# Performance work log

Hardware: AMD Instinct MI355X
Metric: run time of the kernel (lower is better)

## Reference

```python
import jax, jax.numpy as jnp
import numpy as np
from jax import lax

# pywt db5 analysis filter bank (frozen buffers in the torch module)
DEC_LO = np.array([0.003335725285001549, -0.012580751999015526, -0.006241490213011705,
                   0.07757149384006515, -0.03224486958502952, -0.24229488706619015,
                   0.13842814590110342, 0.7243085284385744, 0.6038292697974729,
                   0.160102397974125], dtype=np.float32)
DEC_HI = np.array([-0.160102397974125, 0.6038292697974729, -0.7243085284385744,
                   0.13842814590110342, 0.24229488706619015, -0.03224486958502952,
                   -0.07757149384006515, -0.006241490213011705, 0.012580751999015526,
                   0.003335725285001549], dtype=np.float32)
NUM_LEVELS = 8  # min(round(log2(131072)), max_level=8)


def _conv1d(x, w, padding, lhs_dilation=(1,), groups=1):
    # x: [N, C, L], w: [O, I, K]; cross-correlation, matching torch F.conv1d
    return lax.conv_general_dilated(
        x, w, window_strides=(1,), padding=[padding], lhs_dilation=lhs_dilation,
        dimension_numbers=("NCH", "OIH", "NCH"), feature_group_count=groups)


def setup_inputs() -> dict:
    key = jax.random.key(0)
    k1, k2 = jax.random.split(key)
    x = jax.random.normal(k1, (128, 131072), dtype=jnp.float32)
    # small scale keeps the 8-level synthesis cascade numerically tame
    idwt_filters = jax.random.normal(k2, (128, 8, 2, 32), dtype=jnp.float32) * 0.05
    return {"x": x, "idwt_filters": idwt_filters}


def reference(x, idwt_filters):
    # x: [B, T]; idwt_filters: [B, levels, 2, kw] with kw even
    B, T = x.shape
    w_lo = jnp.asarray(DEC_LO).reshape(1, 1, -1)
    w_hi = jnp.asarray(DEC_HI).reshape(1, 1, -1)
    pad = DEC_LO.shape[0] // 2  # 5 -> conv output length L+1 for kernel 10

    # --- analysis DWT (frozen db5 filters), lengths: T/2^l + 1 per band ---
    lo = x[:, None, :]                       # [B,1,T]
    his = []
    for _ in range(NUM_LEVELS):
        y_lo = _conv1d(lo, w_lo, (pad, pad))
        y_hi = _conv1d(lo, w_hi, (pad, pad))
        lo = y_lo[:, :, ::2]
        his.append(y_hi[:, :, ::2])          # [B,1,T/2^l+1]

    # --- synthesis IDWT with predicted per-example filters (groups=B) ---
    kw = idwt_filters.shape[-1]
    p = kw // 2 - 1
    prev = jnp.transpose(lo, (1, 0, 2))      # [1,B,n]: batch as channels
    for i in range(NUM_LEVELS - 1, -1, -1):
        rec_lo = idwt_filters[:, i, 0, :][:, None, :]   # [B,1,kw]
        rec_hi = idwt_filters[:, i, 1, :][:, None, :]
        hi = jnp.transpose(his[i], (1, 0, 2))           # [1,B,n]
        # lhs_dilation=2 == zero-stuffing even indices; asym pad (p, p+1)
        # reproduces torch's trailing zero at index 2n-1; out length = 2n-1
        y_lo = _conv1d(prev, rec_lo, (p, p + 1), lhs_dilation=(2,), groups=B)
        y_hi = _conv1d(hi, rec_hi, (p, p + 1), lhs_dilation=(2,), groups=B)
        prev = y_lo + y_hi
    return prev[0, :, :-1]                   # [B, T]
```

## Files before the change

### kernel.cpp

```cpp
#include <hip/hip_runtime.h>


static __constant__ float c_dec_lo[10] = {
    0.003335725285001549f, -0.012580751999015526f, -0.006241490213011705f,
    0.07757149384006515f, -0.03224486958502952f, -0.24229488706619015f,
    0.13842814590110342f, 0.7243085284385744f, 0.6038292697974729f,
    0.160102397974125f};
static __constant__ float c_dec_hi[10] = {
    -0.160102397974125f, 0.6038292697974729f, -0.7243085284385744f,
    0.13842814590110342f, 0.24229488706619015f, -0.03224486958502952f,
    -0.07757149384006515f, -0.006241490213011705f, 0.012580751999015526f,
    0.003335725285001549f};

__device__ inline float4 ldz4(const float* __restrict__ row, int j, int L) {
  if (j >= 0 && j + 3 < L) return *reinterpret_cast<const float4*>(row + j);
  float4 r;
  r.x = (j + 0 >= 0 && j + 0 < L) ? row[j + 0] : 0.f;
  r.y = (j + 1 >= 0 && j + 1 < L) ? row[j + 1] : 0.f;
  r.z = (j + 2 >= 0 && j + 2 < L) ? row[j + 2] : 0.f;
  r.w = (j + 3 >= 0 && j + 3 < L) ? row[j + 3] : 0.f;
  return r;
}

__device__ inline void load20(const float* src, int base, float* v) {
#pragma unroll
  for (int q = 0; q < 5; ++q) {
    const float4 t = *reinterpret_cast<const float4*>(src + base + 4 * q);
    v[4 * q + 0] = t.x; v[4 * q + 1] = t.y;
    v[4 * q + 2] = t.z; v[4 * q + 3] = t.w;
  }
}

__device__ inline void load20z(const float* __restrict__ src, int base, int L,
                               float* v) {
#pragma unroll
  for (int q = 0; q < 5; ++q) {
    const float4 t = ldz4(src, base + 4 * q, L);
    v[4 * q + 0] = t.x; v[4 * q + 1] = t.y;
    v[4 * q + 2] = t.z; v[4 * q + 3] = t.w;
  }
}

__device__ inline void load12(const float* src, float* v) {
#pragma unroll
  for (int q = 0; q < 3; ++q) {
    const float4 t = *reinterpret_cast<const float4*>(src + 4 * q);
    v[4 * q + 0] = t.x; v[4 * q + 1] = t.y;
    v[4 * q + 2] = t.z; v[4 * q + 3] = t.w;
  }
}

__device__ inline void fir10x2(const float* v, float* lo, float* hv) {
#pragma unroll
  for (int i = 0; i < 4; ++i) {
    float a = 0.f, h = 0.f;
#pragma unroll
    for (int k = 0; k < 10; ++k) {
      const float xx = v[2 * i + 3 + k];
      a += xx * c_dec_lo[k];
      h += xx * c_dec_hi[k];
    }
    lo[i] = a; hv[i] = h;
  }
}

__device__ inline void fir10x2_split(const float* e, const float* o,
                                     float* lo, float* hv) {
#pragma unroll
  for (int i = 0; i < 4; ++i) {
    float a = 0.f, h = 0.f;
#pragma unroll
    for (int m = 0; m < 5; ++m) {
      const float ov = o[i + 1 + m], ev = e[i + 2 + m];
      a += ov * c_dec_lo[2 * m] + ev * c_dec_lo[2 * m + 1];
      h += ov * c_dec_hi[2 * m] + ev * c_dec_hi[2 * m + 1];
    }
    lo[i] = a; hv[i] = h;
  }
}

__device__ inline void store_hi(float* hg, int A, int idx, const float* hv,
                                int es, int ee) {
  if (idx >= es && idx + 3 < ee) {
    *reinterpret_cast<float4*>(hg + A + idx) =
        make_float4(hv[0], hv[1], hv[2], hv[3]);
  } else {
#pragma unroll
    for (int i = 0; i < 4; ++i)
      if (idx + i >= es && idx + i < ee) hg[A + idx + i] = hv[i];
  }
}

__device__ inline void st4(float* dst, const float* a) {
  *reinterpret_cast<float4*>(dst) = make_float4(a[0], a[1], a[2], a[3]);
}

__device__ inline void store_pad_split(float* E, float* O, int idx,
                                       const float* lo, int vlo, int vhi) {
#pragma unroll
  for (int i = 0; i < 4; ++i) {
    const int s = idx + i;
    const float val = (s >= vlo && s < vhi) ? lo[i] : 0.f;
    if (s & 1) O[s >> 1] = val;
    else E[s >> 1] = val;
  }
}

template <bool FAST>
__device__ inline void fwd_level0(const float* __restrict__ xr, float* E0,
                                  float* O0, float* __restrict__ h0, int A0,
                                  int xoff, int vlo, int vhi, int tid) {
  const int ee = FAST ? 4152 : min(4152, vhi);
  for (int idx = 4 * tid; idx < 4180; idx += 1024) {
    float v[20];
    if (FAST) load20(xr, 2 * idx + xoff, v);
    else load20z(xr, 2 * idx + xoff, 131072, v);
    float lo[4], hv[4];
    fir10x2(v, lo, hv);
    if (FAST) {
      const int j = idx >> 1;
      *reinterpret_cast<float2*>(E0 + j) = make_float2(lo[0], lo[2]);
      *reinterpret_cast<float2*>(O0 + j) = make_float2(lo[1], lo[3]);
      if (idx >= 56 && idx < 4152) st4(h0 + A0 + idx, hv);
    } else {
      store_pad_split(E0, O0, idx, lo, vlo, vhi);
      store_hi(h0, A0, idx, hv, 56, ee);
    }
  }
}

template <bool FAST>
__device__ inline void fwd_levelN(const float* Ein, const float* Oin,
                                  float* Eout, float* Oout,
                                  float* __restrict__ hg, int A, int NOUT,
                                  int esHi, int eeFast, int vlo, int vhi,
                                  int tid) {
  const int ee = FAST ? eeFast : min(eeFast, vhi);
  for (int idx = 4 * tid; idx < NOUT; idx += 1024) {
    float e[12], o[12];
    load12(Ein + idx, e);
    load12(Oin + idx, o);
    float lo[4], hv[4];
    fir10x2_split(e, o, lo, hv);
    if (FAST) {
      const int j = idx >> 1;
      *reinterpret_cast<float2*>(Eout + j) = make_float2(lo[0], lo[2]);
      *reinterpret_cast<float2*>(Oout + j) = make_float2(lo[1], lo[3]);
      if (idx >= esHi && idx < ee) st4(hg + A + idx, hv);
    } else {
      store_pad_split(Eout, Oout, idx, lo, vlo, vhi);
      store_hi(hg, A, idx, hv, esHi, ee);
    }
  }
}

template <bool FAST>
__device__ inline void fwd_level3(const float* Ein, const float* Oin,
                                  float* __restrict__ l3,
                                  float* __restrict__ h3, int b3, int ne3,
                                  int tid) {
  for (int idx = 4 * tid; idx < 512; idx += 1024) {
    float e[12], o[12];
    load12(Ein + idx, e);
    load12(Oin + idx, o);
    float lo[4], hv[4];
    fir10x2_split(e, o, lo, hv);
    if (FAST) {
      st4(l3 + b3 + idx, lo);
      st4(h3 + b3 + idx, hv);
    } else {
      store_hi(l3, b3, idx, lo, 0, ne3);
      store_hi(h3, b3, idx, hv, 0, ne3);
    }
  }
}

__global__ __launch_bounds__(256) void fwd03(
    const float* __restrict__ x, float* __restrict__ hi0,
    float* __restrict__ hi1, float* __restrict__ hi2,
    float* __restrict__ hi3, float* __restrict__ lo3) {
  const int b = blockIdx.y;
  const int bx = blockIdx.x;
  const int b3 = bx * 512;
  __shared__ float E0[2092], O0[2092];
  __shared__ float E1[1044], O1[1044];
  __shared__ float E2[520], O2[520];
  const int tid = threadIdx.x;
  const bool fast = (bx >= 1) && (bx <= 14);
  const float* xr = x + (size_t)b * 131072;
  float* h0 = hi0 + (size_t)b * 65540;
  float* h1 = hi1 + (size_t)b * 32772;
  float* h2 = hi2 + (size_t)b * 16388;
  float* h3 = hi3 + (size_t)b * 8196;
  float* l3 = lo3 + (size_t)b * 8196;
  const int A0 = 8 * b3 - 56, A1 = 4 * b3 - 24, A2 = 2 * b3 - 8;
  const int xoff = 2 * A0 - 8;

  if (fast) {
    fwd_level0<true>(xr, E0, O0, h0, A0, xoff, 0, 0, tid);
    __syncthreads();
    fwd_levelN<true>(E0, O0, E1, O1, h1, A1, 2084, 24, 2072, 0, 0, tid);
    __syncthreads();
    fwd_levelN<true>(E1, O1, E2, O2, h2, A2, 1036, 8, 1032, 0, 0, tid);
    __syncthreads();
    fwd_level3<true>(E2, O2, l3, h3, b3, 512, tid);
  } else {
    fwd_level0<false>(xr, E0, O0, h0, A0, xoff, -A0, 65537 - A0, tid);
    __syncthreads();
    fwd_levelN<false>(E0, O0, E1, O1, h1, A1, 2084, 24, 2072, -A1,
                      32769 - A1, tid);
    __syncthreads();
    fwd_levelN<false>(E1, O1, E2, O2, h2, A2, 1036, 8, 1032, -A2, 16385 - A2,
                      tid);
    __syncthreads();
    fwd_level3<false>(E2, O2, l3, h3, b3, min(512, 8193 - b3), tid);
  }
}

__device__ inline void inv_accum(const float* p, const float* h,
                                 const float4* wpk, float* acc) {
#pragma unroll
  for (int i = 0; i < 8; ++i) acc[i] = 0.f;
#pragma unroll
  for (int m = 0; m < 16; ++m) {
    const float4 w = wpk[m];
#pragma unroll
    for (int e = 0; e < 4; ++e) {
      const float pe = p[e + 1 + m], he = h[e + 1 + m];
      acc[2 * e + 0] += pe * w.y + he * w.w;
      acc[2 * e + 1] += pe * w.x + he * w.z;
    }
  }
}

__global__ __launch_bounds__(256) void inv_big(
    const float* __restrict__ prev, const float* __restrict__ hicoef,
    const float* __restrict__ filt, int level, int L, int sIn, int Tout,
    int sOut, float* __restrict__ out) {
  const int c = blockIdx.y;
  __shared__ float4 wpack[16];
  const int tid = threadIdx.x;
  if (tid < 16) {
    const float* f = filt + ((size_t)c * 8 + level) * 64;
    wpack[tid] = make_float4(f[2 * tid], f[2 * tid + 1],
                             f[32 + 2 * tid], f[32 + 2 * tid + 1]);
  }
  __syncthreads();
  const int g = blockIdx.x * 256 + tid;
  const int t0 = 16 * g;
  if (t0 >= Tout) return;
  const int U = 8 * g - 8;
  const float* prow = prev + (size_t)c * sIn;
  const float* hrow = hicoef + (size_t)c * sIn;
  float p[24], h[24];
  const bool interior = (U >= 0) && (U + 23 < L) && (t0 + 15 < Tout);
  if (interior) {
#pragma unroll
    for (int q = 0; q < 6; ++q) {
      float4 a = *reinterpret_cast<const float4*>(prow + U + 4 * q);
      p[4 * q + 0] = a.x; p[4 * q + 1] = a.y; p[4 * q + 2] = a.z; p[4 * q + 3] = a.w;
      float4 bb = *reinterpret_cast<const float4*>(hrow + U + 4 * q);
      h[4 * q + 0] = bb.x; h[4 * q + 1] = bb.y; h[4 * q + 2] = bb.z; h[4 * q + 3] = bb.w;
    }
  } else {
#pragma unroll
    for (int q = 0; q < 24; ++q) {
      const int j = U + q;
      p[q] = (j >= 0 && j < L) ? prow[j] : 0.f;
      h[q] = (j >= 0 && j < L) ? hrow[j] : 0.f;
    }
  }
  float acc[16];
#pragma unroll
  for (int i = 0; i < 16; ++i) acc[i] = 0.f;
#pragma unroll
  for (int m = 0; m < 16; ++m) {
    const float4 w = wpack[m];
#pragma unroll
    for (int e = 0; e < 8; ++e) {
      const float pv = p[e + 1 + m], hv = h[e + 1 + m];
      acc[2 * e + 0] += pv * w.y + hv * w.w;
      acc[2 * e + 1] += pv * w.x + hv * w.z;
    }
  }
  float* orow = out + (size_t)c * sOut;
  if (interior) {
#pragma unroll
    for (int q = 0; q < 4; ++q)
      *reinterpret_cast<float4*>(orow + t0 + 4 * q) =
          make_float4(acc[4 * q], acc[4 * q + 1], acc[4 * q + 2], acc[4 * q + 3]);
  } else {
#pragma unroll
    for (int i = 0; i < 16; ++i)
      if (t0 + i < Tout) orow[t0 + i] = acc[i];
  }
}

__device__ inline void fwd_tail_level(const float* __restrict__ in,
                                      float* __restrict__ outp, int L, int D,
                                      float* __restrict__ hirow, int tid) {
  for (int d0 = 4 * tid; d0 < D; d0 += 2048) {
    const int jb = 2 * d0 - 8;
    float v[20];
    const bool interior = (jb >= 0) && (jb + 19 < L) && (d0 + 3 < D);
    if (interior) {
      load20(in, jb, v);
    } else {
#pragma unroll
      for (int q = 0; q < 20; ++q) {
        const int j = jb + q;
        v[q] = (j >= 0 && j < L) ? in[j] : 0.f;
      }
    }
    float lo[4], hv[4];
    fir10x2(v, lo, hv);
    if (interior) {
      st4(outp + d0, lo);
      st4(hirow + d0, hv);
    } else {
#pragma unroll
      for (int i = 0; i < 4; ++i)
        if (d0 + i < D) { outp[d0 + i] = lo[i]; hirow[d0 + i] = hv[i]; }
    }
  }
}

__device__ inline void inv_tail_level(const float* __restrict__ pin,
                                      float* __restrict__ pout, int L,
                                      const float* __restrict__ hirow,
                                      const float* __restrict__ filt, int c,
                                      int level, int tid, float4* wpack) {
  __syncthreads();
  if (tid < 16) {
    const float* f = filt + ((size_t)c * 8 + level) * 64;
    wpack[tid] = make_float4(f[2 * tid], f[2 * tid + 1], f[32 + 2 * tid],
                             f[32 + 2 * tid + 1]);
  }
  __syncthreads();
  const int Tout = 2 * L - 1;
  for (int t0 = 8 * tid; t0 < Tout; t0 += 4096) {
    const int U = t0 / 2 - 8;
    float p[20], h[20];
    if (U >= 0 && U + 19 < L) {
      load20(pin, U, p);
      load20(hirow, U, h);
    } else {
#pragma unroll
      for (int q = 0; q < 20; ++q) {
        const int j = U + q;
        p[q] = (j >= 0 && j < L) ? pin[j] : 0.f;
        h[q] = (j >= 0 && j < L) ? hirow[j] : 0.f;
      }
    }
    float acc[8];
    inv_accum(p, h, wpack, acc);
    if (t0 + 7 < Tout) {
      st4(pout + t0, acc);
      st4(pout + t0 + 4, acc + 4);
    } else {
#pragma unroll
      for (int i = 0; i < 8; ++i)
        if (t0 + i < Tout) pout[t0 + i] = acc[i];
    }
  }
}

__global__ __launch_bounds__(512) void mid_fused(
    const float* __restrict__ lo3, const float* __restrict__ filt,
    float* __restrict__ prev3out) {
  const int b = blockIdx.x;
  __shared__ float A[8200];
  __shared__ float Bb[4104];
  __shared__ float H4[4100];
  __shared__ float H5[2052];
  __shared__ float H6[1028];
  __shared__ float H7[516];
  __shared__ float4 wpack[16];
  const int tid = threadIdx.x;
  const float* row = lo3 + (size_t)b * 8196;
  for (int j4 = tid; j4 < 2048; j4 += 512)
    *reinterpret_cast<float4*>(A + 4 * j4) =
        *reinterpret_cast<const float4*>(row + 4 * j4);
  if (tid == 0) A[8192] = row[8192];
  __syncthreads();
  fwd_tail_level(A, Bb, 8193, 4097, H4, tid);
  __syncthreads();
  fwd_tail_level(Bb, A, 4097, 2049, H5, tid);
  __syncthreads();
  fwd_tail_level(A, Bb, 2049, 1025, H6, tid);
  __syncthreads();
  fwd_tail_level(Bb, A, 1025, 513, H7, tid);
  inv_tail_level(A, Bb, 513, H7, filt, b, 7, tid, wpack);
  inv_tail_level(Bb, A, 1025, H6, filt, b, 6, tid, wpack);
  inv_tail_level(A, Bb, 2049, H5, filt, b, 5, tid, wpack);
  inv_tail_level(Bb, prev3out + (size_t)b * 8196, 4097, H4, filt, b, 4, tid,
                 wpack);
}

extern "C" void kernel_launch(void* const* d_in, const int* in_sizes, int n_in,
                              void* d_out, int out_size, void* d_ws,
                              size_t ws_size, hipStream_t stream) {
  const float* x = (const float*)d_in[0];
  const float* filt = (const float*)d_in[1];
  float* out = (float*)d_out;
  float* ws = (float*)d_ws;

  const int B = 128;
  float* lo3buf = ws;
  float* prev3buf = lo3buf + (size_t)B * 8196;
  float* hi0 = prev3buf + (size_t)B * 8196;
  float* hi1 = hi0 + (size_t)B * 65540;
  float* hi2 = hi1 + (size_t)B * 32772;
  float* hi3 = hi2 + (size_t)B * 16388;
  float* prev2buf = hi3 + (size_t)B * 8196;
  float* prev1buf = prev2buf + (size_t)B * 16388;
  float* prev0buf = prev1buf + (size_t)B * 32772;

  hipLaunchKernelGGL(fwd03, dim3(17, B), dim3(256), 0, stream, x, hi0, hi1,
                     hi2, hi3, lo3buf);
  hipLaunchKernelGGL(mid_fused, dim3(B), dim3(512), 0, stream, lo3buf, filt,
                     prev3buf);

  auto launch_inv = [&](const float* prev, const float* hv, int level, int L,
                        int sIn, int Tout, int sOut, float* dst) {
    const int tpr = (Tout + 15) / 16;
    dim3 grid((tpr + 255) / 256, B);
    hipLaunchKernelGGL(inv_big, grid, dim3(256), 0, stream, prev, hv, filt,
                       level, L, sIn, Tout, sOut, dst);
  };
  launch_inv(prev3buf, hi3, 3, 8193, 8196, 16385, 16388, prev2buf);
  launch_inv(prev2buf, hi2, 2, 16385, 16388, 32769, 32772, prev1buf);
  launch_inv(prev1buf, hi1, 1, 32769, 32772, 65537, 65540, prev0buf);
  launch_inv(prev0buf, hi0, 0, 65537, 65540, 131072, 131072, out);
}
```

Measured before the change: 133.4 us.

## Stage input into shared memory and halve forward tile per block

```diff
diff --git a/kernel.cpp b/kernel.cpp
--- a/kernel.cpp
+++ b/kernel.cpp
@@ -31,16 +31,6 @@
   }
 }
 
-__device__ inline void load20z(const float* __restrict__ src, int base, int L,
-                               float* v) {
-#pragma unroll
-  for (int q = 0; q < 5; ++q) {
-    const float4 t = ldz4(src, base + 4 * q, L);
-    v[4 * q + 0] = t.x; v[4 * q + 1] = t.y;
-    v[4 * q + 2] = t.z; v[4 * q + 3] = t.w;
-  }
-}
-
 __device__ inline void load12(const float* src, float* v) {
 #pragma unroll
   for (int q = 0; q < 3; ++q) {
@@ -107,25 +97,14 @@
 }
 
 template <bool FAST>
-__device__ inline void fwd_level0(const float* __restrict__ xr, float* E0,
-                                  float* O0, float* __restrict__ h0, int A0,
-                                  int xoff, int vlo, int vhi, int tid) {
-  const int ee = FAST ? 4152 : min(4152, vhi);
-  for (int idx = 4 * tid; idx < 4180; idx += 1024) {
-    float v[20];
-    if (FAST) load20(xr, 2 * idx + xoff, v);
-    else load20z(xr, 2 * idx + xoff, 131072, v);
-    float lo[4], hv[4];
-    fir10x2(v, lo, hv);
-    if (FAST) {
-      const int j = idx >> 1;
-      *reinterpret_cast<float2*>(E0 + j) = make_float2(lo[0], lo[2]);
-      *reinterpret_cast<float2*>(O0 + j) = make_float2(lo[1], lo[3]);
-      if (idx >= 56 && idx < 4152) st4(h0 + A0 + idx, hv);
-    } else {
-      store_pad_split(E0, O0, idx, lo, vlo, vhi);
-      store_hi(h0, A0, idx, hv, 56, ee);
-    }
+__device__ inline void stage_x(const float* __restrict__ xr, float* Ex,
+                               float* Ox, int xlo, int tid) {
+  for (int u = tid; u < 1069; u += 256) {
+    const float4 v = FAST
+        ? *reinterpret_cast<const float4*>(xr + xlo + 4 * u)
+        : ldz4(xr, xlo + 4 * u, 131072);
+    *reinterpret_cast<float2*>(Ex + 2 * u) = make_float2(v.x, v.z);
+    *reinterpret_cast<float2*>(Ox + 2 * u) = make_float2(v.y, v.w);
   }
 }
 
@@ -159,7 +138,7 @@
                                   float* __restrict__ l3,
                                   float* __restrict__ h3, int b3, int ne3,
                                   int tid) {
-  for (int idx = 4 * tid; idx < 512; idx += 1024) {
+  for (int idx = 4 * tid; idx < 256; idx += 1024) {
     float e[12], o[12];
     load12(Ein + idx, e);
     load12(Oin + idx, o);
@@ -181,12 +160,18 @@
     float* __restrict__ hi3, float* __restrict__ lo3) {
   const int b = blockIdx.y;
   const int bx = blockIdx.x;
-  const int b3 = bx * 512;
-  __shared__ float E0[2092], O0[2092];
-  __shared__ float E1[1044], O1[1044];
-  __shared__ float E2[520], O2[520];
+  const int b3 = bx * 256;
+  __shared__ float W[6416];
+  float* Ex = W;
+  float* Ox = W + 2140;
+  float* E0 = W + 4280;
+  float* O0 = W + 5348;
+  float* E1 = W;
+  float* O1 = W + 532;
+  float* E2 = W + 1064;
+  float* O2 = W + 1328;
   const int tid = threadIdx.x;
-  const bool fast = (bx >= 1) && (bx <= 14);
+  const bool fast = (bx >= 1) && (bx <= 30);
   const float* xr = x + (size_t)b * 131072;
   float* h0 = hi0 + (size_t)b * 65540;
   float* h1 = hi1 + (size_t)b * 32772;
@@ -194,26 +179,31 @@
   float* h3 = hi3 + (size_t)b * 8196;
   float* l3 = lo3 + (size_t)b * 8196;
   const int A0 = 8 * b3 - 56, A1 = 4 * b3 - 24, A2 = 2 * b3 - 8;
-  const int xoff = 2 * A0 - 8;
+  const int xlo = 2 * A0 - 8;
 
   if (fast) {
-    fwd_level0<true>(xr, E0, O0, h0, A0, xoff, 0, 0, tid);
-    __syncthreads();
-    fwd_levelN<true>(E0, O0, E1, O1, h1, A1, 2084, 24, 2072, 0, 0, tid);
-    __syncthreads();
-    fwd_levelN<true>(E1, O1, E2, O2, h2, A2, 1036, 8, 1032, 0, 0, tid);
-    __syncthreads();
-    fwd_level3<true>(E2, O2, l3, h3, b3, 512, tid);
+    stage_x<true>(xr, Ex, Ox, xlo, tid);
+    __syncthreads();
+    fwd_levelN<true>(Ex, Ox, E0, O0, h0, A0, 2132, 56, 2104, 0, 0, tid);
+    __syncthreads();
+    fwd_levelN<true>(E0, O0, E1, O1, h1, A1, 1060, 24, 1048, 0, 0, tid);
+    __syncthreads();
+    fwd_levelN<true>(E1, O1, E2, O2, h2, A2, 524, 8, 520, 0, 0, tid);
+    __syncthreads();
+    fwd_level3<true>(E2, O2, l3, h3, b3, 256, tid);
   } else {
-    fwd_level0<false>(xr, E0, O0, h0, A0, xoff, -A0, 65537 - A0, tid);
-    __syncthreads();
-    fwd_levelN<false>(E0, O0, E1, O1, h1, A1, 2084, 24, 2072, -A1,
+    stage_x<false>(xr, Ex, Ox, xlo, tid);
+    __syncthreads();
+    fwd_levelN<false>(Ex, Ox, E0, O0, h0, A0, 2132, 56, 2104, -A0,
+                      65537 - A0, tid);
+    __syncthreads();
+    fwd_levelN<false>(E0, O0, E1, O1, h1, A1, 1060, 24, 1048, -A1,
                       32769 - A1, tid);
     __syncthreads();
-    fwd_levelN<false>(E1, O1, E2, O2, h2, A2, 1036, 8, 1032, -A2, 16385 - A2,
+    fwd_levelN<false>(E1, O1, E2, O2, h2, A2, 524, 8, 520, -A2, 16385 - A2,
                       tid);
     __syncthreads();
-    fwd_level3<false>(E2, O2, l3, h3, b3, min(512, 8193 - b3), tid);
+    fwd_level3<false>(E2, O2, l3, h3, b3, min(256, 8193 - b3), tid);
   }
 }
 
@@ -416,7 +406,7 @@
   float* prev1buf = prev2buf + (size_t)B * 16388;
   float* prev0buf = prev1buf + (size_t)B * 32772;
 
-  hipLaunchKernelGGL(fwd03, dim3(17, B), dim3(256), 0, stream, x, hi0, hi1,
+  hipLaunchKernelGGL(fwd03, dim3(33, B), dim3(256), 0, stream, x, hi0, hi1,
                      hi2, hi3, lo3buf);
   hipLaunchKernelGGL(mid_fused, dim3(B), dim3(512), 0, stream, lo3buf, filt,
                      prev3buf);
```

New measurement: 134.6 us. About the same (+0.9%).

## Split forward DWT levels 0-3 into independent per-wave tiles with wave-level sync

Applied to the files above, without the earlier changes.

```diff
diff --git a/kernel.cpp b/kernel.cpp
--- a/kernel.cpp
+++ b/kernel.cpp
@@ -106,72 +106,84 @@
   }
 }
 
+__device__ inline void wave_sync() {
+  __builtin_amdgcn_wave_barrier();
+  asm volatile("s_waitcnt lgkmcnt(0)" ::: "memory");
+  __builtin_amdgcn_wave_barrier();
+}
+
 template <bool FAST>
-__device__ inline void fwd_level0(const float* __restrict__ xr, float* E0,
-                                  float* O0, float* __restrict__ h0, int A0,
-                                  int xoff, int vlo, int vhi, int tid) {
-  const int ee = FAST ? 4152 : min(4152, vhi);
-  for (int idx = 4 * tid; idx < 4180; idx += 1024) {
-    float v[20];
-    if (FAST) load20(xr, 2 * idx + xoff, v);
-    else load20z(xr, 2 * idx + xoff, 131072, v);
-    float lo[4], hv[4];
-    fir10x2(v, lo, hv);
-    if (FAST) {
-      const int j = idx >> 1;
-      *reinterpret_cast<float2*>(E0 + j) = make_float2(lo[0], lo[2]);
-      *reinterpret_cast<float2*>(O0 + j) = make_float2(lo[1], lo[3]);
-      if (idx >= 56 && idx < 4152) st4(h0 + A0 + idx, hv);
-    } else {
-      store_pad_split(E0, O0, idx, lo, vlo, vhi);
-      store_hi(h0, A0, idx, hv, 56, ee);
+__device__ inline void wl_level0(const float* __restrict__ xr, float* E0,
+                                 float* O0, float* __restrict__ h0, int A0,
+                                 int xoff, int vlo, int vhi, int eeh,
+                                 int lane) {
+#pragma unroll
+  for (int i = 0; i < 5; ++i) {
+    const int idx = 4 * lane + 256 * i;
+    if (idx < 1108) {
+      float v[20];
+      if (FAST) load20(xr, 2 * idx + xoff, v);
+      else load20z(xr, 2 * idx + xoff, 131072, v);
+      float lo[4], hv[4];
+      fir10x2(v, lo, hv);
+      if (FAST) {
+        const int j = idx >> 1;
+        *reinterpret_cast<float2*>(E0 + j) = make_float2(lo[0], lo[2]);
+        *reinterpret_cast<float2*>(O0 + j) = make_float2(lo[1], lo[3]);
+        if (idx >= 56 && idx < 1080) st4(h0 + A0 + idx, hv);
+      } else {
+        store_pad_split(E0, O0, idx, lo, vlo, vhi);
+        store_hi(h0, A0, idx, hv, 56, eeh);
+      }
     }
   }
 }
 
 template <bool FAST>
-__device__ inline void fwd_levelN(const float* Ein, const float* Oin,
-                                  float* Eout, float* Oout,
-                                  float* __restrict__ hg, int A, int NOUT,
-                                  int esHi, int eeFast, int vlo, int vhi,
-                                  int tid) {
-  const int ee = FAST ? eeFast : min(eeFast, vhi);
-  for (int idx = 4 * tid; idx < NOUT; idx += 1024) {
-    float e[12], o[12];
-    load12(Ein + idx, e);
-    load12(Oin + idx, o);
-    float lo[4], hv[4];
-    fir10x2_split(e, o, lo, hv);
-    if (FAST) {
-      const int j = idx >> 1;
-      *reinterpret_cast<float2*>(Eout + j) = make_float2(lo[0], lo[2]);
-      *reinterpret_cast<float2*>(Oout + j) = make_float2(lo[1], lo[3]);
-      if (idx >= esHi && idx < ee) st4(hg + A + idx, hv);
-    } else {
-      store_pad_split(Eout, Oout, idx, lo, vlo, vhi);
-      store_hi(hg, A, idx, hv, esHi, ee);
+__device__ inline void wl_levelN(const float* Ein, const float* Oin,
+                                 float* Eout, float* Oout,
+                                 float* __restrict__ hg, int A, int NOUT,
+                                 int iters, int esHi, int eeHiF, int vlo,
+                                 int vhi, int lane) {
+  for (int i = 0; i < iters; ++i) {
+    const int idx = 4 * lane + 256 * i;
+    if (idx < NOUT) {
+      float e[12], o[12];
+      load12(Ein + idx, e);
+      load12(Oin + idx, o);
+      float lo[4], hv[4];
+      fir10x2_split(e, o, lo, hv);
+      if (FAST) {
+        const int j = idx >> 1;
+        *reinterpret_cast<float2*>(Eout + j) = make_float2(lo[0], lo[2]);
+        *reinterpret_cast<float2*>(Oout + j) = make_float2(lo[1], lo[3]);
+        if (idx >= esHi && idx < eeHiF) st4(hg + A + idx, hv);
+      } else {
+        store_pad_split(Eout, Oout, idx, lo, vlo, vhi);
+        store_hi(hg, A, idx, hv, esHi, min(eeHiF, vhi));
+      }
     }
   }
 }
 
 template <bool FAST>
-__device__ inline void fwd_level3(const float* Ein, const float* Oin,
-                                  float* __restrict__ l3,
-                                  float* __restrict__ h3, int b3, int ne3,
-                                  int tid) {
-  for (int idx = 4 * tid; idx < 512; idx += 1024) {
-    float e[12], o[12];
-    load12(Ein + idx, e);
-    load12(Oin + idx, o);
-    float lo[4], hv[4];
-    fir10x2_split(e, o, lo, hv);
-    if (FAST) {
-      st4(l3 + b3 + idx, lo);
-      st4(h3 + b3 + idx, hv);
-    } else {
-      store_hi(l3, b3, idx, lo, 0, ne3);
-      store_hi(h3, b3, idx, hv, 0, ne3);
-    }
+__device__ inline void wl_level3(const float* Ein, const float* Oin,
+                                 float* __restrict__ l3,
+                                 float* __restrict__ h3, int T, int ne3,
+                                 int lane) {
+  const int idx = 4 * lane;
+  if (idx >= 128) return;
+  float e[12], o[12];
+  load12(Ein + idx, e);
+  load12(Oin + idx, o);
+  float lo[4], hv[4];
+  fir10x2_split(e, o, lo, hv);
+  if (FAST) {
+    st4(l3 + T + idx, lo);
+    st4(h3 + T + idx, hv);
+  } else {
+    store_hi(l3, T, idx, lo, 0, ne3);
+    store_hi(h3, T, idx, hv, 0, ne3);
   }
 }
 
@@ -180,40 +192,46 @@
     float* __restrict__ hi1, float* __restrict__ hi2,
     float* __restrict__ hi3, float* __restrict__ lo3) {
   const int b = blockIdx.y;
-  const int bx = blockIdx.x;
-  const int b3 = bx * 512;
-  __shared__ float E0[2092], O0[2092];
-  __shared__ float E1[1044], O1[1044];
-  __shared__ float E2[520], O2[520];
-  const int tid = threadIdx.x;
-  const bool fast = (bx >= 1) && (bx <= 14);
+  const int widx = threadIdx.x >> 6;
+  const int lane = threadIdx.x & 63;
+  const int gw = blockIdx.x * 4 + widx;
+  __shared__ float W[7744];
+  float* E0 = W + widx * 1936;
+  float* O0 = E0 + 556;
+  float* E1 = O0 + 556;
+  float* O1 = E1 + 276;
+  float* E2 = O1 + 276;
+  float* O2 = E2 + 136;
+  if (gw > 64) return;
+  const int T = gw * 128;
   const float* xr = x + (size_t)b * 131072;
   float* h0 = hi0 + (size_t)b * 65540;
   float* h1 = hi1 + (size_t)b * 32772;
   float* h2 = hi2 + (size_t)b * 16388;
   float* h3 = hi3 + (size_t)b * 8196;
   float* l3 = lo3 + (size_t)b * 8196;
-  const int A0 = 8 * b3 - 56, A1 = 4 * b3 - 24, A2 = 2 * b3 - 8;
-  const int xoff = 2 * A0 - 8;
-
-  if (fast) {
-    fwd_level0<true>(xr, E0, O0, h0, A0, xoff, 0, 0, tid);
-    __syncthreads();
-    fwd_levelN<true>(E0, O0, E1, O1, h1, A1, 2084, 24, 2072, 0, 0, tid);
-    __syncthreads();
-    fwd_levelN<true>(E1, O1, E2, O2, h2, A2, 1036, 8, 1032, 0, 0, tid);
-    __syncthreads();
-    fwd_level3<true>(E2, O2, l3, h3, b3, 512, tid);
+  const int A0 = 8 * T - 56, A1 = 4 * T - 24, A2 = 2 * T - 8;
+  const int xoff = 16 * T - 120;
+
+  if (gw >= 1 && gw <= 62) {
+    wl_level0<true>(xr, E0, O0, h0, A0, xoff, 0, 0, 0, lane);
+    wave_sync();
+    wl_levelN<true>(E0, O0, E1, O1, h1, A1, 548, 3, 24, 536, 0, 0, lane);
+    wave_sync();
+    wl_levelN<true>(E1, O1, E2, O2, h2, A2, 268, 2, 8, 264, 0, 0, lane);
+    wave_sync();
+    wl_level3<true>(E2, O2, l3, h3, T, 128, lane);
   } else {
-    fwd_level0<false>(xr, E0, O0, h0, A0, xoff, -A0, 65537 - A0, tid);
-    __syncthreads();
-    fwd_levelN<false>(E0, O0, E1, O1, h1, A1, 2084, 24, 2072, -A1,
-                      32769 - A1, tid);
-    __syncthreads();
-    fwd_levelN<false>(E1, O1, E2, O2, h2, A2, 1036, 8, 1032, -A2, 16385 - A2,
-                      tid);
-    __syncthreads();
-    fwd_level3<false>(E2, O2, l3, h3, b3, min(512, 8193 - b3), tid);
+    wl_level0<false>(xr, E0, O0, h0, A0, xoff, (A0 < 0) ? -A0 : 0,
+                     min(1108, 65537 - A0), min(1080, 65537 - A0), lane);
+    wave_sync();
+    wl_levelN<false>(E0, O0, E1, O1, h1, A1, 548, 3, 24, 536,
+                     (A1 < 0) ? -A1 : 0, min(548, 32769 - A1), lane);
+    wave_sync();
+    wl_levelN<false>(E1, O1, E2, O2, h2, A2, 268, 2, 8, 264,
+                     (A2 < 0) ? -A2 : 0, min(268, 16385 - A2), lane);
+    wave_sync();
+    wl_level3<false>(E2, O2, l3, h3, T, min(128, 8193 - T), lane);
   }
 }
 
```

Result: no change. 132.8 us (-0.4%).
